# Optimization experiments

Measured on AMD Instinct MI355X. Metric: run time of the kernel, lower is better.

The kernel has to match this reference:

```python
import jax, jax.numpy as jnp
import numpy as np

MAX_DISP = 24   # maxDisp = 192/8
K = 3           # box-filter kernel size
PAD = 1         # conv padding


def _cost_volume(inputs):
    # inputs: [B, 2c, H, W]; first half is input1, second half is input2
    b, c2, h, w = inputs.shape
    c = c2 // 2
    x1 = inputs[:, :c]
    x2 = inputs[:, c:]
    # pad input2 on the left by MAX_DISP (matches Fun.pad(..., (max_disp,0,0,0)))
    x2p = jnp.pad(x2, ((0, 0), (0, 0), (0, 0), (MAX_DISP, 0)))
    # original loop: d = MAX_DISP .. 0, slice [d:d+w]; output channel i uses
    # d = MAX_DISP - i, i.e. input2 shifted right by i pixels.
    slices = [
        jnp.einsum('bchw,bchw->bhw', x1,
                   x2p[:, :, :, MAX_DISP - i:MAX_DISP - i + w])
        for i in range(MAX_DISP + 1)
    ]
    corr = jnp.stack(slices, axis=1)  # [B, D+1, H, W]
    # per-channel (depthwise) conv with an all-ones KxK kernel == original
    # single-channel conv2d applied to each disparity slice
    ones = jnp.ones((MAX_DISP + 1, 1, K, K), dtype=inputs.dtype)
    out = jax.lax.conv_general_dilated(
        corr, ones,
        window_strides=(1, 1),
        padding=((PAD, PAD), (PAD, PAD)),
        feature_group_count=MAX_DISP + 1,
        dimension_numbers=('NCHW', 'OIHW', 'NCHW'))
    return out  # [B, MAX_DISP+1, H, W]


def setup_inputs() -> dict:
    key = jax.random.key(0)
    inputs = jax.random.normal(key, (16, 512, 64, 192), dtype=jnp.float32)
    return {"inputs": inputs}


def reference(inputs):
    return _cost_volume(inputs)
```

## Files before the change

kernel.cpp:

```cpp
#include <hip/hip_runtime.h>

constexpr int Bq = 16;
constexpr int Cc = 256;
constexpr int Hh = 64;
constexpr int Ww = 192;
constexpr int Dd = 25;
constexpr int HW = Hh * Ww;
constexpr int BSTRIDE = 2 * Cc * HW;
constexpr int CPR = 4;
constexpr int NS = 4;
constexpr int CS = Cc / NS;
constexpr int NR = CS / CPR;
constexpr int ROWP = 24 + Ww;
constexpr size_t PLANE = (size_t)Bq * Dd * Hh * Ww;

__global__ __launch_bounds__(192) void corr_kernel(const float* __restrict__ in,
                                                   float* __restrict__ part) {
  const int t   = threadIdx.x;
  const int hg  = blockIdx.x;
  const int b   = blockIdx.y;
  const int s   = blockIdx.z;
  const int row = t / 96;
  const int u   = t % 96;
  const int w0  = 2 * u;
  const int h   = hg * 2 + row;

  __shared__ float x2s[2][CPR][ROWP];

  {
    const int r2  = t / (CPR * 24);
    const int rem = t % (CPR * 24);
    x2s[r2][rem / 24][rem % 24] = 0.0f;
  }

  const float* x1p = in + (size_t)b * BSTRIDE + (size_t)(s * CS) * HW
                        + (size_t)h * Ww + w0;
  const float* x2p = x1p + (size_t)Cc * HW;

  float2 acc[Dd];
#pragma unroll
  for (int d = 0; d < Dd; ++d) acc[d] = make_float2(0.0f, 0.0f);

  float2 px1[CPR], px2[CPR];
#pragma unroll
  for (int c = 0; c < CPR; ++c) {
    px1[c] = *(const float2*)(x1p + c * HW);
    px2[c] = *(const float2*)(x2p + c * HW);
  }

  for (int rnd = 0; rnd < NR; ++rnd) {
    __syncthreads();
    float2 cx1[CPR];
#pragma unroll
    for (int c = 0; c < CPR; ++c) {
      cx1[c] = px1[c];
      *(float2*)&x2s[row][c][24 + w0] = px2[c];
    }
    __syncthreads();

    if (rnd + 1 < NR) {
      const float* p1 = x1p + (size_t)(rnd + 1) * CPR * HW;
      const float* p2 = p1 + (size_t)Cc * HW;
#pragma unroll
      for (int c = 0; c < CPR; ++c) {
        px1[c] = *(const float2*)(p1 + c * HW);
        px2[c] = *(const float2*)(p2 + c * HW);
      }
    }

#pragma unroll
    for (int c = 0; c < CPR; ++c) {
      float win[26];
#pragma unroll
      for (int k = 0; k < 13; ++k) {
        const float2 v = *(const float2*)&x2s[row][c][w0 + 2 * k];
        win[2 * k]     = v.x;
        win[2 * k + 1] = v.y;
      }
      const float a0 = cx1[c].x, a1 = cx1[c].y;
#pragma unroll
      for (int d = 0; d < Dd; ++d) {
        acc[d].x = fmaf(a0, win[24 - d], acc[d].x);
        acc[d].y = fmaf(a1, win[25 - d], acc[d].y);
      }
    }
  }

  float* cp = part + s * PLANE + ((size_t)b * Dd * Hh + h) * Ww + w0;
#pragma unroll
  for (int d = 0; d < Dd; ++d)
    *(float2*)(cp + (size_t)d * HW) = acc[d];
}

__global__ __launch_bounds__(192) void box_kernel(const float* __restrict__ part,
                                                  float* __restrict__ out) {
  const int w  = threadIdx.x;
  const int h  = blockIdx.x;
  const int bd = blockIdx.y;

  __shared__ float v[Ww + 2];
  if (w == 0)  v[0] = 0.0f;
  if (w == 1)  v[Ww + 1] = 0.0f;

  float sum = 0.0f;
#pragma unroll
  for (int si = 0; si < NS; ++si) {
    const float* base = part + si * PLANE + ((size_t)bd * Hh + h) * Ww;
#pragma unroll
    for (int dh = -1; dh <= 1; ++dh) {
      const int hh = h + dh;
      if (hh >= 0 && hh < Hh) sum += base[(size_t)dh * Ww + w];
    }
  }
  v[w + 1] = sum;
  __syncthreads();
  out[((size_t)bd * Hh + h) * Ww + w] = v[w] + v[w + 1] + v[w + 2];
}

extern "C" void kernel_launch(void* const* d_in, const int* in_sizes, int n_in,
                              void* d_out, int out_size, void* d_ws, size_t ws_size,
                              hipStream_t stream) {
  const float* in = (const float*)d_in[0];
  float* out  = (float*)d_out;
  float* part = (float*)d_ws;

  dim3 g1(Hh / 2, Bq, NS);
  corr_kernel<<<g1, 192, 0, stream>>>(in, part);

  dim3 g2(Hh, Bq * Dd);
  box_kernel<<<g2, Ww, 0, stream>>>(part, out);
}
```

Baseline: 591.6 us.

## Restructure correlation into single-wave blocks with double-buffered LDS and fewer splits

The correlation kernel now uses one 64-thread wavefront per block, one row per block. Each active lane computes four adjacent pixels with float4 accumulators. Channel groups are prefetched two steps ahead into double-buffered shared memory, with no block barriers because the block is a single wave. The channel split drops from four to two, which halves the partial-plane writes and reads. The box filter now walks 32 rows per block with a rolling three-row window, so each partial row is read once instead of three times. The trade-offs are that a quarter of the lanes in the correlation wave do no compute, and fewer, smaller blocks give less latency hiding.

```diff
diff --git a/kernel.cpp b/kernel.cpp
--- a/kernel.cpp
+++ b/kernel.cpp
@@ -1,120 +1,152 @@
 #include <hip/hip_runtime.h>
 
-constexpr int Bq = 16;
-constexpr int Cc = 256;
-constexpr int Hh = 64;
-constexpr int Ww = 192;
-constexpr int Dd = 25;
+constexpr int Bq = 16, Cc = 256, Hh = 64, Ww = 192, Dd = 25;
 constexpr int HW = Hh * Ww;
 constexpr int BSTRIDE = 2 * Cc * HW;
-constexpr int CPR = 4;
-constexpr int NS = 4;
+constexpr int NS = 2;
 constexpr int CS = Cc / NS;
-constexpr int NR = CS / CPR;
+constexpr int GC = 4;
+constexpr int NG = CS / GC;
 constexpr int ROWP = 24 + Ww;
 constexpr size_t PLANE = (size_t)Bq * Dd * Hh * Ww;
 
-__global__ __launch_bounds__(192) void corr_kernel(const float* __restrict__ in,
-                                                   float* __restrict__ part) {
-  const int t   = threadIdx.x;
-  const int hg  = blockIdx.x;
-  const int b   = blockIdx.y;
-  const int s   = blockIdx.z;
-  const int row = t / 96;
-  const int u   = t % 96;
-  const int w0  = 2 * u;
-  const int h   = hg * 2 + row;
+__global__ __launch_bounds__(64, 2) void corr_kernel(const float* __restrict__ in,
+                                                     float* __restrict__ part) {
+  const int t = threadIdx.x;
+  const int h = blockIdx.x;
+  const int b = blockIdx.y;
+  const int s = blockIdx.z;
 
-  __shared__ float x2s[2][CPR][ROWP];
+  __shared__ float x2s[2][GC][ROWP];
 
-  {
-    const int r2  = t / (CPR * 24);
-    const int rem = t % (CPR * 24);
-    x2s[r2][rem / 24][rem % 24] = 0.0f;
+#pragma unroll
+  for (int i = 0; i < 3; ++i) {
+    const int idx  = i * 64 + t;
+    const int slot = idx / (GC * 24);
+    const int rem  = idx % (GC * 24);
+    x2s[slot][rem / 24][rem % 24] = 0.0f;
   }
 
-  const float* x1p = in + (size_t)b * BSTRIDE + (size_t)(s * CS) * HW
-                        + (size_t)h * Ww + w0;
-  const float* x2p = x1p + (size_t)Cc * HW;
+  const float* x1row = in + (size_t)b * BSTRIDE + (size_t)(s * CS) * HW
+                          + (size_t)h * Ww;
+  const float* x2row = x1row + (size_t)Cc * HW;
 
-  float2 acc[Dd];
+  const bool comp = (t < 48);
+  const int  w0   = 4 * t;
+
+  float4 acc[Dd];
 #pragma unroll
-  for (int d = 0; d < Dd; ++d) acc[d] = make_float2(0.0f, 0.0f);
+  for (int d = 0; d < Dd; ++d) acc[d] = make_float4(0.f, 0.f, 0.f, 0.f);
 
-  float2 px1[CPR], px2[CPR];
+  float  px2[2][GC][3];
+  float4 px1[2][GC];
+
 #pragma unroll
-  for (int c = 0; c < CPR; ++c) {
-    px1[c] = *(const float2*)(x1p + c * HW);
-    px2[c] = *(const float2*)(x2p + c * HW);
+  for (int gen = 0; gen < 2; ++gen) {
+    const float* b2 = x2row + (size_t)(gen * GC) * HW;
+#pragma unroll
+    for (int c = 0; c < GC; ++c)
+#pragma unroll
+      for (int k = 0; k < 3; ++k)
+        px2[gen][c][k] = b2[(size_t)c * HW + 64 * k + t];
+    if (comp) {
+      const float* b1 = x1row + (size_t)(gen * GC) * HW;
+#pragma unroll
+      for (int c = 0; c < GC; ++c)
+        px1[gen][c] = *(const float4*)(b1 + (size_t)c * HW + w0);
+    }
+  }
+#pragma unroll
+  for (int c = 0; c < GC; ++c)
+#pragma unroll
+    for (int k = 0; k < 3; ++k)
+      x2s[0][c][24 + 64 * k + t] = px2[0][c][k];
+
+#define STEP(g, GS)                                                          \
+  {                                                                          \
+    if ((g) + 1 < NG) {                                                      \
+      _Pragma("unroll")                                                      \
+      for (int c = 0; c < GC; ++c)                                           \
+        _Pragma("unroll")                                                    \
+        for (int k = 0; k < 3; ++k)                                          \
+          x2s[1 - (GS)][c][24 + 64 * k + t] = px2[1 - (GS)][c][k];           \
+    }                                                                        \
+    if ((g) + 2 < NG) {                                                      \
+      const float* b2 = x2row + (size_t)(((g) + 2) * GC) * HW;               \
+      _Pragma("unroll")                                                      \
+      for (int c = 0; c < GC; ++c)                                           \
+        _Pragma("unroll")                                                    \
+        for (int k = 0; k < 3; ++k)                                          \
+          px2[GS][c][k] = b2[(size_t)c * HW + 64 * k + t];                   \
+    }                                                                        \
+    if (comp) {                                                              \
+      _Pragma("unroll")                                                      \
+      for (int c = 0; c < GC; ++c) {                                         \
+        float win[28];                                                       \
+        _Pragma("unroll")                                                    \
+        for (int k = 0; k < 7; ++k)                                          \
+          *(float4*)&win[4 * k] = *(const float4*)&x2s[GS][c][w0 + 4 * k];   \
+        const float4 a = px1[GS][c];                                         \
+        _Pragma("unroll")                                                    \
+        for (int d = 0; d < Dd; ++d) {                                       \
+          acc[d].x = fmaf(a.x, win[24 - d], acc[d].x);                       \
+          acc[d].y = fmaf(a.y, win[25 - d], acc[d].y);                       \
+          acc[d].z = fmaf(a.z, win[26 - d], acc[d].z);                       \
+          acc[d].w = fmaf(a.w, win[27 - d], acc[d].w);                       \
+        }                                                                    \
+      }                                                                      \
+      if ((g) + 2 < NG) {                                                    \
+        const float* b1 = x1row + (size_t)(((g) + 2) * GC) * HW;             \
+        _Pragma("unroll")                                                    \
+        for (int c = 0; c < GC; ++c)                                         \
+          px1[GS][c] = *(const float4*)(b1 + (size_t)c * HW + w0);           \
+      }                                                                      \
+    }                                                                        \
   }
 
-  for (int rnd = 0; rnd < NR; ++rnd) {
-    __syncthreads();
-    float2 cx1[CPR];
+  for (int g = 0; g < NG; g += 2) {
+    STEP(g, 0)
+    STEP(g + 1, 1)
+  }
+#undef STEP
+
+  if (comp) {
+    float* cp = part + (size_t)s * PLANE + ((size_t)b * Dd * Hh + h) * Ww + w0;
 #pragma unroll
-    for (int c = 0; c < CPR; ++c) {
-      cx1[c] = px1[c];
-      *(float2*)&x2s[row][c][24 + w0] = px2[c];
-    }
-    __syncthreads();
-
-    if (rnd + 1 < NR) {
-      const float* p1 = x1p + (size_t)(rnd + 1) * CPR * HW;
-      const float* p2 = p1 + (size_t)Cc * HW;
-#pragma unroll
-      for (int c = 0; c < CPR; ++c) {
-        px1[c] = *(const float2*)(p1 + c * HW);
-        px2[c] = *(const float2*)(p2 + c * HW);
-      }
-    }
-
-#pragma unroll
-    for (int c = 0; c < CPR; ++c) {
-      float win[26];
-#pragma unroll
-      for (int k = 0; k < 13; ++k) {
-        const float2 v = *(const float2*)&x2s[row][c][w0 + 2 * k];
-        win[2 * k]     = v.x;
-        win[2 * k + 1] = v.y;
-      }
-      const float a0 = cx1[c].x, a1 = cx1[c].y;
-#pragma unroll
-      for (int d = 0; d < Dd; ++d) {
-        acc[d].x = fmaf(a0, win[24 - d], acc[d].x);
-        acc[d].y = fmaf(a1, win[25 - d], acc[d].y);
-      }
-    }
+    for (int d = 0; d < Dd; ++d)
+      *(float4*)(cp + (size_t)d * HW) = acc[d];
   }
-
-  float* cp = part + s * PLANE + ((size_t)b * Dd * Hh + h) * Ww + w0;
-#pragma unroll
-  for (int d = 0; d < Dd; ++d)
-    *(float2*)(cp + (size_t)d * HW) = acc[d];
 }
 
 __global__ __launch_bounds__(192) void box_kernel(const float* __restrict__ part,
                                                   float* __restrict__ out) {
-  const int w  = threadIdx.x;
-  const int h  = blockIdx.x;
-  const int bd = blockIdx.y;
+  const int w    = threadIdx.x;
+  const int half = blockIdx.x;
+  const int bd   = blockIdx.y;
+  const int h0   = half * 32;
+
+  const float* p0 = part + (size_t)bd * Hh * Ww;
+  const float* p1 = p0 + PLANE;
 
   __shared__ float v[Ww + 2];
-  if (w == 0)  v[0] = 0.0f;
-  if (w == 1)  v[Ww + 1] = 0.0f;
+  if (w == 0) v[0] = 0.f;
+  if (w == 1) v[Ww + 1] = 0.f;
 
-  float sum = 0.0f;
-#pragma unroll
-  for (int si = 0; si < NS; ++si) {
-    const float* base = part + si * PLANE + ((size_t)bd * Hh + h) * Ww;
-#pragma unroll
-    for (int dh = -1; dh <= 1; ++dh) {
-      const int hh = h + dh;
-      if (hh >= 0 && hh < Hh) sum += base[(size_t)dh * Ww + w];
-    }
+  auto loadrow = [&](int hh) -> float {
+    if (hh < 0 || hh >= Hh) return 0.f;
+    return p0[(size_t)hh * Ww + w] + p1[(size_t)hh * Ww + w];
+  };
+
+  float rp = loadrow(h0 - 1);
+  float rc = loadrow(h0);
+  for (int h = h0; h < h0 + 32; ++h) {
+    const float rn = loadrow(h + 1);
+    __syncthreads();
+    v[w + 1] = rp + rc + rn;
+    __syncthreads();
+    out[((size_t)bd * Hh + h) * Ww + w] = v[w] + v[w + 1] + v[w + 2];
+    rp = rc; rc = rn;
   }
-  v[w + 1] = sum;
-  __syncthreads();
-  out[((size_t)bd * Hh + h) * Ww + w] = v[w] + v[w + 1] + v[w + 2];
 }
 
 extern "C" void kernel_launch(void* const* d_in, const int* in_sizes, int n_in,
@@ -124,9 +156,9 @@
   float* out  = (float*)d_out;
   float* part = (float*)d_ws;
 
-  dim3 g1(Hh / 2, Bq, NS);
-  corr_kernel<<<g1, 192, 0, stream>>>(in, part);
+  dim3 g1(Hh, Bq, NS);
+  corr_kernel<<<g1, 64, 0, stream>>>(in, part);
 
-  dim3 g2(Hh, Bq * Dd);
-  box_kernel<<<g2, Ww, 0, stream>>>(part, out);
+  dim3 g2(2, Bq * Dd);
+  box_kernel<<<g2, 192, 0, stream>>>(part, out);
 }
```

Result: slower. 790.8 us (+33.7%).
